# Optimization experiments

Hardware: AMD Instinct MI355X
Metric: run time of the kernel (lower is better)

Reference implementation:

```python
import jax, jax.numpy as jnp
import numpy as np

SCALE = 0.125  # 1/sqrt(d_k), d_k = 64


def setup_inputs() -> dict:
    key = jax.random.key(0)
    kq, kk, kv, kp = jax.random.split(key, 4)
    H, B, L, T, D = 16, 4, 1024, 1024, 64
    return {
        "query": jax.random.normal(kq, (H, B, L, D), dtype=jnp.float32),
        "key": jax.random.normal(kk, (H, B, T, D), dtype=jnp.float32),
        "value": jax.random.normal(kv, (H, B, T, D), dtype=jnp.float32),
        "prev_attention": jax.random.normal(kp, (H, B, L, T), dtype=jnp.float32),
    }


def reference(query, key, value, prev_attention):
    # scores: [h, b, l, t]
    scores = jnp.einsum("hblk,hbtk->hblt", query, key) * SCALE
    scores = scores + prev_attention
    attention = jax.nn.softmax(scores, axis=-1)
    # dropout disabled (rate 0.0) for deterministic reference
    output = jnp.einsum("hblt,hbtv->hblv", attention, value)
    return (output, attention)
```

## Files before the change

kernel.cpp:

```cpp
#include <hip/hip_runtime.h>

#define SCALE 0.125f

constexpr int L_ = 1024, T_ = 1024, D_ = 64, HB_ = 64, QB = 16;

using f32x4 = __attribute__((ext_vector_type(4))) float;
using half8 = __attribute__((ext_vector_type(8))) _Float16;
using half4 = __attribute__((ext_vector_type(4))) _Float16;

__global__ __launch_bounds__(256, 3) void attn_fused(
    const float* __restrict__ q, const float* __restrict__ kk,
    const float* __restrict__ vv, const float* __restrict__ prev,
    float* __restrict__ out, float* __restrict__ att) {
  __shared__ __align__(16) _Float16 El[QB][1032];
  __shared__ __align__(16) _Float16 Ks[64][72];
  __shared__ __align__(16) _Float16 Vt[64][72];
  __shared__ float zb[4][16];

  const int ltile = blockIdx.x;
  const int hb    = blockIdx.y;
  const int tid = threadIdx.x;
  const int w = tid >> 6, l = tid & 63, l15 = l & 15, lg = l >> 4;
  const int qrow = ltile * QB + l15;

  half8 qb2[2];
  {
    const float* qp = q + ((size_t)hb * L_ + qrow) * D_ + lg * 8;
#pragma unroll
    for (int f = 0; f < 2; ++f)
#pragma unroll
      for (int e = 0; e < 8; ++e) qb2[f][e] = (_Float16)qp[f * 32 + e];
  }

  const float* prow =
      prev + ((size_t)hb * L_ + qrow) * (size_t)T_ + w * 16 + lg * 4;
  const float* kbase = kk + (size_t)hb * T_ * D_;
  const float* vbase = vv + (size_t)hb * T_ * D_;

  const int sr = tid >> 2;
  const int sc = (tid & 3) * 16;
  const int dj = (tid & 3) * 4;

  float4 kq[4], vq[4];
  auto kload = [&](int c) {
    const float* p = kbase + (size_t)(c * 64 + sr) * D_ + sc;
#pragma unroll
    for (int i = 0; i < 4; ++i) kq[i] = *(const float4*)(p + i * 4);
  };
  auto vload = [&](int c) {
    const float* p = vbase + (size_t)(c * 64 + sr) * D_;
#pragma unroll
    for (int i = 0; i < 4; ++i) vq[i] = *(const float4*)(p + i * 16 + dj);
  };
  auto kwrite = [&]() {
    half8 h0, h1;
    const float* f0 = (const float*)&kq[0];
    const float* f1 = (const float*)&kq[2];
#pragma unroll
    for (int e = 0; e < 8; ++e) { h0[e] = (_Float16)f0[e]; h1[e] = (_Float16)f1[e]; }
    *(half8*)&Ks[sr][sc] = h0;
    *(half8*)&Ks[sr][sc + 8] = h1;
  };
  auto vwrite = [&]() {
#pragma unroll
    for (int i = 0; i < 4; ++i) {
      Vt[i * 16 + dj + 0][sr] = (_Float16)vq[i].x;
      Vt[i * 16 + dj + 1][sr] = (_Float16)vq[i].y;
      Vt[i * 16 + dj + 2][sr] = (_Float16)vq[i].z;
      Vt[i * 16 + dj + 3][sr] = (_Float16)vq[i].w;
    }
  };

  f32x4 pb[2];
  auto pload = [&](int c) { pb[c & 1] = *(const f32x4*)(prow + c * 64); };

  kload(0); vload(0); pload(0);
  kwrite(); vwrite();

  float zsum = 0.f;
  f32x4 oacc = {0.f, 0.f, 0.f, 0.f};

#pragma unroll 4
  for (int c = 0; c < 16; ++c) {
    __syncthreads();
    f32x4 pv = pb[c & 1];
    if (c < 15) { kload(c + 1); vload(c + 1); pload(c + 1); }

    const int trow = w * 16 + l15;
    half8 ka0 = *(const half8*)&Ks[trow][lg * 8];
    half8 ka1 = *(const half8*)&Ks[trow][32 + lg * 8];
    f32x4 acc = {0.f, 0.f, 0.f, 0.f};
    acc = __builtin_amdgcn_mfma_f32_16x16x32_f16(ka0, qb2[0], acc, 0, 0, 0);
    acc = __builtin_amdgcn_mfma_f32_16x16x32_f16(ka1, qb2[1], acc, 0, 0, 0);

    float e0 = __expf(acc[0] * SCALE + pv[0]);
    float e1 = __expf(acc[1] * SCALE + pv[1]);
    float e2 = __expf(acc[2] * SCALE + pv[2]);
    float e3 = __expf(acc[3] * SCALE + pv[3]);
    zsum += (e0 + e1) + (e2 + e3);
    half4 ev;
    ev[0] = (_Float16)e0; ev[1] = (_Float16)e1;
    ev[2] = (_Float16)e2; ev[3] = (_Float16)e3;
    *(half4*)&El[l15][c * 64 + w * 16 + lg * 4] = ev;

    __syncthreads();

#pragma unroll
    for (int ks = 0; ks < 2; ++ks) {
      half8 ea = *(const half8*)&El[l15][c * 64 + ks * 32 + lg * 8];
      half8 vb = *(const half8*)&Vt[w * 16 + l15][ks * 32 + lg * 8];
      oacc = __builtin_amdgcn_mfma_f32_16x16x32_f16(ea, vb, oacc, 0, 0, 0);
    }

    __syncthreads();
    if (c < 15) { kwrite(); vwrite(); }
  }

  zsum += __shfl_xor(zsum, 16, 64);
  zsum += __shfl_xor(zsum, 32, 64);
  if (lg == 0) zb[w][l15] = zsum;
  __syncthreads();

  {
    float* ob = out + ((size_t)hb * L_ + ltile * QB) * (size_t)D_;
#pragma unroll
    for (int i = 0; i < 4; ++i) {
      const int qq = lg * 4 + i;
      float z = (zb[0][qq] + zb[1][qq]) + (zb[2][qq] + zb[3][qq]);
      ob[(size_t)qq * D_ + w * 16 + l15] = oacc[i] / z;
    }
  }

  {
    const int row = tid >> 4, tc = tid & 15;
    const float z =
        (zb[0][row] + zb[1][row]) + (zb[2][row] + zb[3][row]);
    const float rzr = 1.0f / z;
    float* attw =
        att + ((size_t)hb * L_ + ltile * QB + row) * (size_t)T_ + tc * 4;
    const _Float16* ep = &El[row][tc * 4];
#pragma unroll
    for (int j = 0; j < 16; ++j) {
      half4 ev = *(const half4*)(ep + j * 64);
      f32x4 s = {(float)ev[0] * rzr, (float)ev[1] * rzr,
                 (float)ev[2] * rzr, (float)ev[3] * rzr};
      *(f32x4*)(attw + j * 64) = s;
    }
  }
}

extern "C" void kernel_launch(void* const* d_in, const int* in_sizes, int n_in,
                              void* d_out, int out_size, void* d_ws,
                              size_t ws_size, hipStream_t stream) {
  const float* q    = (const float*)d_in[0];
  const float* k    = (const float*)d_in[1];
  const float* v    = (const float*)d_in[2];
  const float* prev = (const float*)d_in[3];

  float* out = (float*)d_out;
  float* att = out + (size_t)HB_ * L_ * D_;

  dim3 grid(L_ / QB, HB_);
  attn_fused<<<grid, 256, 0, stream>>>(q, k, v, prev, out, att);
}
```

Baseline: 242.4 us.

## Deepen K/V/prev prefetch, drop mid-loop barrier via per-wave PV partials

K, V and prev_attention loads are now prefetched two chunks ahead into double-buffered registers. The P·V MFMA now takes each wave's own freshly computed exp values, zero-padded to the k=32 operand width, so the barrier between the exp store and the PV step is gone. Each wave keeps four output accumulators. These are reduced across waves through shared memory that aliases the K/V tiles, then written as coalesced float4 stores. In exchange, half of each PV MFMA is wasted on zero padding, and register pressure rises under the 3-waves-per-SIMD launch bound, which could cause spills.

```diff
diff --git a/kernel.cpp b/kernel.cpp
--- a/kernel.cpp
+++ b/kernel.cpp
@@ -13,9 +13,12 @@
     const float* __restrict__ vv, const float* __restrict__ prev,
     float* __restrict__ out, float* __restrict__ att) {
   __shared__ __align__(16) _Float16 El[QB][1032];
-  __shared__ __align__(16) _Float16 Ks[64][72];
-  __shared__ __align__(16) _Float16 Vt[64][72];
+  __shared__ __align__(16) unsigned char KV[18432];
   __shared__ float zb[4][16];
+
+  auto Ks  = (_Float16(*)[72])KV;
+  auto Vt  = (_Float16(*)[72])(KV + 9216);
+  auto ob4 = (float(*)[16][72])KV;
 
   const int ltile = blockIdx.x;
   const int hb    = blockIdx.y;
@@ -41,50 +44,59 @@
   const int sc = (tid & 3) * 16;
   const int dj = (tid & 3) * 4;
 
-  float4 kq[4], vq[4];
-  auto kload = [&](int c) {
+  float4 kq[2][4], vq[2][4];
+  f32x4 pbv[2];
+  auto kload = [&](int c, int s) {
     const float* p = kbase + (size_t)(c * 64 + sr) * D_ + sc;
 #pragma unroll
-    for (int i = 0; i < 4; ++i) kq[i] = *(const float4*)(p + i * 4);
+    for (int i = 0; i < 4; ++i) kq[s][i] = *(const float4*)(p + i * 4);
   };
-  auto vload = [&](int c) {
+  auto vload = [&](int c, int s) {
     const float* p = vbase + (size_t)(c * 64 + sr) * D_;
 #pragma unroll
-    for (int i = 0; i < 4; ++i) vq[i] = *(const float4*)(p + i * 16 + dj);
+    for (int i = 0; i < 4; ++i) vq[s][i] = *(const float4*)(p + i * 16 + dj);
   };
-  auto kwrite = [&]() {
+  auto pload = [&](int c, int s) { pbv[s] = *(const f32x4*)(prow + c * 64); };
+  auto kwrite = [&](int s) {
     half8 h0, h1;
-    const float* f0 = (const float*)&kq[0];
-    const float* f1 = (const float*)&kq[2];
+    const float* f0 = (const float*)&kq[s][0];
+    const float* f1 = (const float*)&kq[s][2];
 #pragma unroll
-    for (int e = 0; e < 8; ++e) { h0[e] = (_Float16)f0[e]; h1[e] = (_Float16)f1[e]; }
+    for (int e = 0; e < 8; ++e) {
+      h0[e] = (_Float16)f0[e];
+      h1[e] = (_Float16)f1[e];
+    }
     *(half8*)&Ks[sr][sc] = h0;
     *(half8*)&Ks[sr][sc + 8] = h1;
   };
-  auto vwrite = [&]() {
+  auto vwrite = [&](int s) {
 #pragma unroll
     for (int i = 0; i < 4; ++i) {
-      Vt[i * 16 + dj + 0][sr] = (_Float16)vq[i].x;
-      Vt[i * 16 + dj + 1][sr] = (_Float16)vq[i].y;
-      Vt[i * 16 + dj + 2][sr] = (_Float16)vq[i].z;
-      Vt[i * 16 + dj + 3][sr] = (_Float16)vq[i].w;
+      Vt[i * 16 + dj + 0][sr] = (_Float16)vq[s][i].x;
+      Vt[i * 16 + dj + 1][sr] = (_Float16)vq[s][i].y;
+      Vt[i * 16 + dj + 2][sr] = (_Float16)vq[s][i].z;
+      Vt[i * 16 + dj + 3][sr] = (_Float16)vq[s][i].w;
     }
   };
 
-  f32x4 pb[2];
-  auto pload = [&](int c) { pb[c & 1] = *(const f32x4*)(prow + c * 64); };
-
-  kload(0); vload(0); pload(0);
-  kwrite(); vwrite();
+  kload(0, 0); vload(0, 0); pload(0, 0);
+  kwrite(0); vwrite(0);
+  kload(1, 1); vload(1, 1); pload(1, 1);
 
   float zsum = 0.f;
-  f32x4 oacc = {0.f, 0.f, 0.f, 0.f};
+  f32x4 oacc[4];
+#pragma unroll
+  for (int nd = 0; nd < 4; ++nd) oacc[nd] = (f32x4){0.f, 0.f, 0.f, 0.f};
 
-#pragma unroll 4
+#pragma unroll 2
   for (int c = 0; c < 16; ++c) {
     __syncthreads();
-    f32x4 pv = pb[c & 1];
-    if (c < 15) { kload(c + 1); vload(c + 1); pload(c + 1); }
+    f32x4 pv = pbv[c & 1];
+    if (c < 14) {
+      kload(c + 2, c & 1);
+      vload(c + 2, c & 1);
+      pload(c + 2, c & 1);
+    }
 
     const int trow = w * 16 + l15;
     half8 ka0 = *(const half8*)&Ks[trow][lg * 8];
@@ -103,32 +115,45 @@
     ev[2] = (_Float16)e2; ev[3] = (_Float16)e3;
     *(half4*)&El[l15][c * 64 + w * 16 + lg * 4] = ev;
 
-    __syncthreads();
-
+    half8 af;
+    af[0] = ev[0]; af[1] = ev[1]; af[2] = ev[2]; af[3] = ev[3];
+    af[4] = af[5] = af[6] = af[7] = (_Float16)0.f;
 #pragma unroll
-    for (int ks = 0; ks < 2; ++ks) {
-      half8 ea = *(const half8*)&El[l15][c * 64 + ks * 32 + lg * 8];
-      half8 vb = *(const half8*)&Vt[w * 16 + l15][ks * 32 + lg * 8];
-      oacc = __builtin_amdgcn_mfma_f32_16x16x32_f16(ea, vb, oacc, 0, 0, 0);
+    for (int nd = 0; nd < 4; ++nd) {
+      half4 v4 = *(const half4*)&Vt[nd * 16 + l15][w * 16 + lg * 4];
+      half8 vb;
+      vb[0] = v4[0]; vb[1] = v4[1]; vb[2] = v4[2]; vb[3] = v4[3];
+      vb[4] = vb[5] = vb[6] = vb[7] = (_Float16)0.f;
+      oacc[nd] = __builtin_amdgcn_mfma_f32_16x16x32_f16(af, vb, oacc[nd], 0, 0, 0);
     }
 
     __syncthreads();
-    if (c < 15) { kwrite(); vwrite(); }
+    if (c < 15) { kwrite((c + 1) & 1); vwrite((c + 1) & 1); }
   }
 
   zsum += __shfl_xor(zsum, 16, 64);
   zsum += __shfl_xor(zsum, 32, 64);
   if (lg == 0) zb[w][l15] = zsum;
+
+#pragma unroll
+  for (int nd = 0; nd < 4; ++nd)
+#pragma unroll
+    for (int i = 0; i < 4; ++i)
+      ob4[w][lg * 4 + i][nd * 16 + l15] = oacc[nd][i];
   __syncthreads();
 
   {
-    float* ob = out + ((size_t)hb * L_ + ltile * QB) * (size_t)D_;
-#pragma unroll
-    for (int i = 0; i < 4; ++i) {
-      const int qq = lg * 4 + i;
-      float z = (zb[0][qq] + zb[1][qq]) + (zb[2][qq] + zb[3][qq]);
-      ob[(size_t)qq * D_ + w * 16 + l15] = oacc[i] / z;
-    }
+    const int qq = tid >> 4, dd = (tid & 15) * 4;
+    const float z =
+        (zb[0][qq] + zb[1][qq]) + (zb[2][qq] + zb[3][qq]);
+    const float rzq = 1.0f / z;
+    f32x4 o0 = *(const f32x4*)&ob4[0][qq][dd];
+    f32x4 o1 = *(const f32x4*)&ob4[1][qq][dd];
+    f32x4 o2 = *(const f32x4*)&ob4[2][qq][dd];
+    f32x4 o3 = *(const f32x4*)&ob4[3][qq][dd];
+    f32x4 o = ((o0 + o1) + (o2 + o3));
+    o[0] *= rzq; o[1] *= rzq; o[2] *= rzq; o[3] *= rzq;
+    *(f32x4*)(out + ((size_t)hb * L_ + ltile * QB + qq) * (size_t)D_ + dd) = o;
   }
 
   {
```

After: 250.4 us. +3.3%, slower.
